# Optimization experiments

Hardware: AMD Instinct MI355X
Metric: run time of the kernel (lower is better)

## Reference

```python
import jax, jax.numpy as jnp
import numpy as np

DIM = 128
HEADS = 4
HD = DIM // HEADS  # 32
WS = 8             # search window (ws x ws candidates)
K = 16             # top-k neighbors kept
SCALE = HD ** -0.5


def _sepconv(x, w_dw, w_pw, b):
    # depthwise 3x3 ('SAME', reflect-free) + pointwise 1x1 with bias (SepConv2d)
    C = x.shape[1]
    y = jax.lax.conv_general_dilated(x, w_dw, (1, 1), 'SAME',
                                     feature_group_count=C,
                                     dimension_numbers=('NCHW', 'OIHW', 'NCHW'))
    return jnp.einsum('bchw,oc->bohw', y, w_pw) + b[None, :, None, None]


def _refl(i, n):
    # dnls reflect_bounds: mirror indices back into [0, n-1]
    i = jnp.where(i < 0, -i, i)
    return jnp.where(i >= n, 2 * (n - 1) - i, i)


def _neighbor_idx(T, H, W, ws):
    # flat pixel index of the ws*ws spatial candidates per query (wt=0: same frame)
    off = jnp.arange(ws) - ws // 2
    ni = _refl(jnp.arange(H)[:, None] + off[None, :], H)  # [H,ws]
    nj = _refl(jnp.arange(W)[:, None] + off[None, :], W)  # [W,ws]
    pix = ni[:, None, :, None] * W + nj[None, :, None, :]  # [H,W,ws,ws]
    idx = jnp.arange(T)[:, None, None, None, None] * (H * W) + pix[None]
    return idx.reshape(T * H * W, ws * ws).astype(jnp.int32)  # [Q,L]


def reference(vid, wq_dw, wq_pw, bq, wk_dw, wk_pw, bk, wv_dw, wv_pw, bv, proj_w, proj_b):
    B, T, C, H, W = vid.shape
    Q = T * H * W
    x = vid.reshape(B * T, C, H, W)
    # qkv conv projection; q pre-scaled as in get_qkv
    q = _sepconv(x, wq_dw, wq_pw, bq) * SCALE
    k = _sepconv(x, wk_dw, wk_pw, bk)
    v = _sepconv(x, wv_dw, wv_pw, bv)

    def heads(z):  # [B*T,C,H,W] -> [B,heads,Q,hd]
        return z.reshape(B, T, HEADS, HD, H, W).transpose(0, 2, 1, 4, 5, 3).reshape(B, HEADS, Q, HD)

    qh, kh, vh = heads(q), heads(k), heads(v)
    idx = _neighbor_idx(T, H, W, WS)            # [Q,L]
    kg = jnp.take(kh, idx, axis=2)              # [B,h,Q,L,hd] irregular gather
    dists = jnp.einsum('bhqd,bhqld->bhql', qh, kg)
    vals, args = jax.lax.top_k(dists, K)        # k-NN by prod distance
    attn = jax.nn.softmax(vals, axis=-1)        # run_softmax over k
    sel = jnp.take_along_axis(jnp.broadcast_to(idx[None, None], (B, HEADS) + idx.shape), args, axis=-1)
    vsel = jnp.take_along_axis(vh, sel.reshape(B, HEADS, Q * K)[..., None], axis=2).reshape(B, HEADS, Q, K, HD)
    out = jnp.einsum('bhqk,bhqkd->bhqd', attn, vsel)   # wpsum (ps=pt=1)
    out = out.transpose(0, 2, 1, 3).reshape(B, Q, C)   # merge heads: (h c)
    y = out @ proj_w.T + proj_b                        # nn.Linear proj
    # fold: ps=1, stride0=1 -> zvid==1, pure reshape back to video
    return y.reshape(B, T, H, W, C).transpose(0, 1, 4, 2, 3)


def setup_inputs() -> dict:
    key = jax.random.key(0)
    ks = jax.random.split(key, 12)
    s = 0.02
    return {
        'vid': jax.random.normal(ks[0], (1, 2, DIM, 96, 96), jnp.float32),
        'wq_dw': jax.random.normal(ks[1], (DIM, 1, 3, 3), jnp.float32) * s,
        'wq_pw': jax.random.normal(ks[2], (DIM, DIM), jnp.float32) * s,
        'bq': jax.random.normal(ks[3], (DIM,), jnp.float32) * s,
        'wk_dw': jax.random.normal(ks[4], (DIM, 1, 3, 3), jnp.float32) * s,
        'wk_pw': jax.random.normal(ks[5], (DIM, DIM), jnp.float32) * s,
        'bk': jax.random.normal(ks[6], (DIM,), jnp.float32) * s,
        'wv_dw': jax.random.normal(ks[7], (DIM, 1, 3, 3), jnp.float32) * s,
        'wv_pw': jax.random.normal(ks[8], (DIM, DIM), jnp.float32) * s,
        'bv': jax.random.normal(ks[9], (DIM,), jnp.float32) * s,
        'proj_w': jax.random.normal(ks[10], (DIM, DIM), jnp.float32) * s,
        'proj_b': jax.random.normal(ks[11], (DIM,), jnp.float32) * s,
    }
```

## Files before the change

### kernel.cpp

```cpp
#include <hip/hip_runtime.h>
#include <math.h>

#define TT 2
#define CH 128
#define HH 96
#define WW 96
#define HWS 9216
#define QTOT 18432
#define QC (QTOT*CH)
#define HD 32
#define KTOP 16
#define SCALE 0.17677669529663687f

#define SEG 16
#define PR 8
#define PC 23
#define PSTRIDE 36

typedef __attribute__((ext_vector_type(8))) short short8;
typedef __attribute__((ext_vector_type(4))) float floatx4;

__device__ __forceinline__ unsigned short f2bf(float f) {
    union { float f; unsigned u; } x; x.f = f;
    unsigned r = x.u + 0x7fffu + ((x.u >> 16) & 1u);
    return (unsigned short)(r >> 16);
}
__device__ __forceinline__ float bf2f(unsigned short h) {
    return __uint_as_float(((unsigned)h) << 16);
}

__device__ __forceinline__ int refl(int x, int n) {
    x = x < 0 ? -x : x;
    return x >= n ? 2 * (n - 1) - x : x;
}

__global__ __launch_bounds__(256) void dwcvt_kernel(
    const float* __restrict__ x,
    const float* __restrict__ wq, const float* __restrict__ wk, const float* __restrict__ wv,
    unsigned short* __restrict__ qk_hi,
    unsigned short* __restrict__ qk_lo,
    unsigned short* __restrict__ v_bf)
{
    int t = threadIdx.x;
    int pl = t & 63;
    int cg = __builtin_amdgcn_readfirstlane(t >> 6);
    int p  = blockIdx.x * 64 + pl;
    int c0 = blockIdx.y * 32 + cg * 8;
    int hw = p % HWS;
    int tt = p / HWS;
    int i = hw / WW, j = hw % WW;

    unsigned qh[4], ql[4], kh[4], kl[4], vh4[4];
#pragma unroll
    for (int ic = 0; ic < 8; ic += 2) {
        float sv[3][2];
#pragma unroll
        for (int u = 0; u < 2; u++) {
            int c = c0 + ic + u;
            const float* xp = x + (size_t)(tt * CH + c) * HWS;
            float w0[9], w1[9], w2[9];
#pragma unroll
            for (int r = 0; r < 9; r++) {
                w0[r] = wq[c * 9 + r]; w1[r] = wk[c * 9 + r]; w2[r] = wv[c * 9 + r];
            }
            float s0 = 0.f, s1 = 0.f, s2 = 0.f;
#pragma unroll
            for (int r = 0; r < 3; r++) {
                int ii = i + r - 1;
                if (ii < 0 || ii >= HH) continue;
#pragma unroll
                for (int ss = 0; ss < 3; ss++) {
                    int jj = j + ss - 1;
                    if (jj < 0 || jj >= WW) continue;
                    float xv = xp[ii * WW + jj];
                    s0 += xv * w0[r * 3 + ss];
                    s1 += xv * w1[r * 3 + ss];
                    s2 += xv * w2[r * 3 + ss];
                }
            }
            sv[0][u] = s0; sv[1][u] = s1; sv[2][u] = s2;
        }
        int w = ic >> 1;
        unsigned short h0 = f2bf(sv[0][0]), h1 = f2bf(sv[0][1]);
        qh[w] = h0 | ((unsigned)h1 << 16);
        ql[w] = f2bf(sv[0][0] - bf2f(h0)) | ((unsigned)f2bf(sv[0][1] - bf2f(h1)) << 16);
        h0 = f2bf(sv[1][0]); h1 = f2bf(sv[1][1]);
        kh[w] = h0 | ((unsigned)h1 << 16);
        kl[w] = f2bf(sv[1][0] - bf2f(h0)) | ((unsigned)f2bf(sv[1][1] - bf2f(h1)) << 16);
        vh4[w] = f2bf(sv[2][0]) | ((unsigned)f2bf(sv[2][1]) << 16);
    }
    size_t off = (size_t)p * CH + c0;
    uint4 pk;
    pk.x = qh[0]; pk.y = qh[1]; pk.z = qh[2]; pk.w = qh[3];
    *(uint4*)(qk_hi + off) = pk;
    pk.x = ql[0]; pk.y = ql[1]; pk.z = ql[2]; pk.w = ql[3];
    *(uint4*)(qk_lo + off) = pk;
    pk.x = kh[0]; pk.y = kh[1]; pk.z = kh[2]; pk.w = kh[3];
    *(uint4*)(qk_hi + (size_t)QC + off) = pk;
    pk.x = kl[0]; pk.y = kl[1]; pk.z = kl[2]; pk.w = kl[3];
    *(uint4*)(qk_lo + (size_t)QC + off) = pk;
    pk.x = vh4[0]; pk.y = vh4[1]; pk.z = vh4[2]; pk.w = vh4[3];
    *(uint4*)(v_bf + off) = pk;
}

__global__ __launch_bounds__(256) void qkv_mfma(
    const unsigned short* __restrict__ Ahi,
    const unsigned short* __restrict__ Alo,
    const unsigned short* __restrict__ Avb,
    const float* __restrict__ wq_pw, const float* __restrict__ wk_pw,
    const float* __restrict__ wv_pw,
    const float* __restrict__ bq, const float* __restrict__ bk, const float* __restrict__ bv,
    float* __restrict__ qkf,
    unsigned short* __restrict__ vh)
{
    __shared__ unsigned short WhS[128 * 136];
    __shared__ unsigned short WlS[128 * 136];
    int sel = blockIdx.y;
    int t = threadIdx.x;
    int wv = t >> 6, lane = t & 63;
    int m = lane & 15, quad = lane >> 4;
    int p0 = blockIdx.x * 64;
    int o0 = wv * 32;

    if (sel == 2) {
#pragma unroll
        for (int r = 0; r < 16; r++) {
            int lin = r * 256 + t;
            int o = lin >> 5, cq = lin & 31;
            float4 w4 = *(const float4*)(wv_pw + o * CH + cq * 4);
            uint2 pk;
            pk.x = f2bf(w4.x) | ((unsigned)f2bf(w4.y) << 16);
            pk.y = f2bf(w4.z) | ((unsigned)f2bf(w4.w) << 16);
            *(uint2*)(&WhS[o * 136 + cq * 4]) = pk;
        }
        __syncthreads();
        float bb[2];
#pragma unroll
        for (int ot = 0; ot < 2; ot++) bb[ot] = bv[o0 + ot * 16 + m];
        floatx4 acc[4][2];
#pragma unroll
        for (int i = 0; i < 4; i++)
#pragma unroll
            for (int j = 0; j < 2; j++) acc[i][j] = (floatx4){0.f, 0.f, 0.f, 0.f};
#pragma unroll
        for (int kc = 0; kc < 4; kc++) {
            short8 a[4], b[2];
#pragma unroll
            for (int pt = 0; pt < 4; pt++)
                a[pt] = *(const short8*)(Avb + (size_t)(p0 + pt * 16 + m) * CH + kc * 32 + quad * 8);
#pragma unroll
            for (int ot = 0; ot < 2; ot++)
                b[ot] = *(const short8*)(&WhS[(o0 + ot * 16 + m) * 136 + kc * 32 + quad * 8]);
#pragma unroll
            for (int pt = 0; pt < 4; pt++)
#pragma unroll
                for (int ot = 0; ot < 2; ot++)
                    acc[pt][ot] = __builtin_amdgcn_mfma_f32_16x16x32_bf16(a[pt], b[ot], acc[pt][ot], 0, 0, 0);
        }
        unsigned short* vhh = vh + (size_t)wv * QTOT * 32;
#pragma unroll
        for (int pt = 0; pt < 4; pt++)
#pragma unroll
            for (int ot = 0; ot < 2; ot++)
#pragma unroll
                for (int reg = 0; reg < 4; reg++) {
                    int p = p0 + pt * 16 + quad * 4 + reg;
                    vhh[(size_t)p * 32 + ot * 16 + m] = f2bf(acc[pt][ot][reg] + bb[ot]);
                }
        return;
    }

    const float* W = sel ? wk_pw : wq_pw;
    const float* bias = sel ? bk : bq;
    float scale = sel ? 1.f : SCALE;
    const unsigned short* ah = Ahi + (size_t)sel * QC;
    const unsigned short* al = Alo + (size_t)sel * QC;
    float* O = qkf + (size_t)sel * QC;

#pragma unroll
    for (int r = 0; r < 16; r++) {
        int lin = r * 256 + t;
        int o = lin >> 5, cq = lin & 31;
        float4 w4 = *(const float4*)(W + o * CH + cq * 4);
        unsigned short hx = f2bf(w4.x), hy = f2bf(w4.y), hz = f2bf(w4.z), hw = f2bf(w4.w);
        unsigned short lx = f2bf(w4.x - bf2f(hx)), ly = f2bf(w4.y - bf2f(hy));
        unsigned short lz = f2bf(w4.z - bf2f(hz)), lw = f2bf(w4.w - bf2f(hw));
        uint2 pk;
        pk.x = hx | ((unsigned)hy << 16); pk.y = hz | ((unsigned)hw << 16);
        *(uint2*)(&WhS[o * 136 + cq * 4]) = pk;
        pk.x = lx | ((unsigned)ly << 16); pk.y = lz | ((unsigned)lw << 16);
        *(uint2*)(&WlS[o * 136 + cq * 4]) = pk;
    }
    __syncthreads();
    float bb[2];
#pragma unroll
    for (int ot = 0; ot < 2; ot++) bb[ot] = bias[o0 + ot * 16 + m];
    floatx4 acc[4][2];
#pragma unroll
    for (int i = 0; i < 4; i++)
#pragma unroll
        for (int j = 0; j < 2; j++) acc[i][j] = (floatx4){0.f, 0.f, 0.f, 0.f};
#pragma unroll
    for (int kc = 0; kc < 4; kc++) {
        short8 avh[4], avl[4], bh[2], bl[2];
#pragma unroll
        for (int pt = 0; pt < 4; pt++) {
            size_t base = (size_t)(p0 + pt * 16 + m) * CH + kc * 32 + quad * 8;
            avh[pt] = *(const short8*)(ah + base);
            avl[pt] = *(const short8*)(al + base);
        }
#pragma unroll
        for (int ot = 0; ot < 2; ot++) {
            int lidx = (o0 + ot * 16 + m) * 136 + kc * 32 + quad * 8;
            bh[ot] = *(const short8*)(&WhS[lidx]);
            bl[ot] = *(const short8*)(&WlS[lidx]);
        }
#pragma unroll
        for (int pt = 0; pt < 4; pt++)
#pragma unroll
            for (int ot = 0; ot < 2; ot++) {
                acc[pt][ot] = __builtin_amdgcn_mfma_f32_16x16x32_bf16(avh[pt], bh[ot], acc[pt][ot], 0, 0, 0);
                acc[pt][ot] = __builtin_amdgcn_mfma_f32_16x16x32_bf16(avh[pt], bl[ot], acc[pt][ot], 0, 0, 0);
                acc[pt][ot] = __builtin_amdgcn_mfma_f32_16x16x32_bf16(avl[pt], bh[ot], acc[pt][ot], 0, 0, 0);
            }
    }
#pragma unroll
    for (int pt = 0; pt < 4; pt++)
#pragma unroll
        for (int ot = 0; ot < 2; ot++)
#pragma unroll
            for (int reg = 0; reg < 4; reg++) {
                int p = p0 + pt * 16 + quad * 4 + reg;
                O[(size_t)p * CH + o0 + ot * 16 + m] = (acc[pt][ot][reg] + bb[ot]) * scale;
            }
}

__global__ __launch_bounds__(256) void attn_kernel(
    const float* __restrict__ q,
    const float* __restrict__ k,
    const unsigned short* __restrict__ vh,
    unsigned short* __restrict__ att)
{
    __shared__ float kp[PR * PC * PSTRIDE];
    int h = blockIdx.y;
    int n = blockIdx.x;
    int seg = (n & 7) * 144 + (n >> 3);
    int qj0 = (seg % (WW / SEG)) * SEG;
    int qi = (seg / (WW / SEG)) % HH;
    int tt = seg / ((WW / SEG) * HH);
    int t = threadIdx.x;

#pragma unroll
    for (int r = 0; r < 6; r++) {
        int f = r * 256 + t;
        if (f < PR * PC * 8) {
            int pix = f >> 3, d4 = f & 7;
            int ci = pix / PC, cj = pix - ci * PC;
            int gi = refl(qi + ci - 4, HH);
            int gj = refl(qj0 + cj - 4, WW);
            int gp = tt * HWS + gi * WW + gj;
            *(float4*)(&kp[pix * PSTRIDE + d4 * 4]) =
                *(const float4*)(k + (size_t)gp * CH + h * HD + d4 * 4);
        }
    }
    __syncthreads();

    int wv = t >> 6, lane = t & 63;
    int ci = lane >> 3, cjo = lane & 7;
    int di = ci - 4, dj = cjo - 4;
    int rowoff = tt * HWS + refl(qi + di, HH) * WW;
    const int d = lane & (HD - 1);
    const unsigned long long below = (1ull << lane) - 1ull;
    const unsigned short* vhh = vh + (size_t)h * QTOT * 32;

    for (int ql = wv * 4; ql < wv * 4 + 4; ql++) {
        int qj = qj0 + ql;
        int p = tt * HWS + qi * WW + qj;
        const float* qp = q + (size_t)p * CH + h * HD;
        const float* kr = &kp[(ci * PC + ql + cjo) * PSTRIDE];
        float dist = 0.f;
#pragma unroll
        for (int dd = 0; dd < 8; dd++) {
            float4 qv = *(const float4*)(qp + dd * 4);
            float4 kv = *(const float4*)(kr + dd * 4);
            dist += qv.x * kv.x + qv.y * kv.y + qv.z * kv.z + qv.w * kv.w;
        }
        int cpix = rowoff + refl(qj + dj, WW);

        unsigned u = __float_as_uint(dist);
        unsigned key = (u & 0x80000000u) ? ~u : (u | 0x80000000u);

        unsigned prefix = 0u;
        int need = KTOP;
#pragma unroll
        for (int bit = 31; bit >= 0; --bit) {
            unsigned hi = (prefix >> bit) | 1u;
            unsigned long long b = __ballot((key >> bit) == hi);
            int cnt = __popcll(b);
            bool take = cnt >= need;
            prefix = take ? (prefix | (1u << bit)) : prefix;
            need = take ? need : need - cnt;
        }
        bool isEq = (key == prefix);
        unsigned long long eqm = __ballot(isEq);
        int rk = __popcll(eqm & below);
        bool selb = (key > prefix) || (isEq && rk < need);
        unsigned long long selm = __ballot(selb);

        float e = selb ? __expf(dist) : 0.f;

        float acc = 0.f, denom = 0.f;
        unsigned long long m0 = selm;
#pragma unroll
        for (int r = 0; r < KTOP; r++) {
            int s0 = __builtin_ctzll(m0); m0 &= m0 - 1ull;
            float a0 = __uint_as_float((unsigned)__builtin_amdgcn_readlane((int)__float_as_uint(e), s0));
            int pr = __builtin_amdgcn_readlane(cpix, s0);
            denom += a0;
            acc += a0 * bf2f(vhh[(size_t)pr * 32 + d]);
        }
        if (lane < HD)
            att[(size_t)p * CH + h * HD + lane] = f2bf(acc / denom);
    }
}

__global__ __launch_bounds__(256) void proj_mfma(
    const unsigned short* __restrict__ A,
    const float* __restrict__ W,
    const float* __restrict__ bias,
    float* __restrict__ out)
{
    __shared__ unsigned short Ws[128 * 136];
    int t = threadIdx.x;
#pragma unroll
    for (int r = 0; r < 16; r++) {
        int lin = r * 256 + t;
        int o = lin >> 5, cq = lin & 31;
        float4 w4 = *(const float4*)(W + o * CH + cq * 4);
        uint2 pk;
        pk.x = f2bf(w4.x) | ((unsigned)f2bf(w4.y) << 16);
        pk.y = f2bf(w4.z) | ((unsigned)f2bf(w4.w) << 16);
        *(uint2*)(&Ws[o * 136 + cq * 4]) = pk;
    }
    __syncthreads();
    int wv = t >> 6, lane = t & 63;
    int m = lane & 15, quad = lane >> 4;
    int p0 = blockIdx.x * 64;
    int o0 = wv * 32;
    float bb[2][4];
#pragma unroll
    for (int ot = 0; ot < 2; ot++)
#pragma unroll
        for (int reg = 0; reg < 4; reg++) bb[ot][reg] = bias[o0 + ot * 16 + quad * 4 + reg];
    floatx4 acc[2][4];
#pragma unroll
    for (int i = 0; i < 2; i++)
#pragma unroll
        for (int j = 0; j < 4; j++) acc[i][j] = (floatx4){0.f, 0.f, 0.f, 0.f};
#pragma unroll
    for (int kc = 0; kc < 4; kc++) {
        short8 a[2], b[4];
#pragma unroll
        for (int ot = 0; ot < 2; ot++)
            a[ot] = *(const short8*)(&Ws[(o0 + ot * 16 + m) * 136 + kc * 32 + quad * 8]);
#pragma unroll
        for (int pt = 0; pt < 4; pt++)
            b[pt] = *(const short8*)(A + (size_t)(p0 + pt * 16 + m) * CH + kc * 32 + quad * 8);
#pragma unroll
        for (int ot = 0; ot < 2; ot++)
#pragma unroll
            for (int pt = 0; pt < 4; pt++)
                acc[ot][pt] = __builtin_amdgcn_mfma_f32_16x16x32_bf16(a[ot], b[pt], acc[ot][pt], 0, 0, 0);
    }
    int tt = p0 / HWS;
    int hwb = p0 - tt * HWS;
#pragma unroll
    for (int ot = 0; ot < 2; ot++)
#pragma unroll
        for (int pt = 0; pt < 4; pt++)
#pragma unroll
            for (int reg = 0; reg < 4; reg++) {
                int o = o0 + ot * 16 + quad * 4 + reg;
                int hw = hwb + pt * 16 + m;
                out[((size_t)(tt * CH + o)) * HWS + hw] = acc[ot][pt][reg] + bb[ot][reg];
            }
}

extern "C" void kernel_launch(void* const* d_in, const int* in_sizes, int n_in,
                              void* d_out, int out_size, void* d_ws, size_t ws_size,
                              hipStream_t stream) {
    const float* vid    = (const float*)d_in[0];
    const float* wq_dw  = (const float*)d_in[1];
    const float* wq_pw  = (const float*)d_in[2];
    const float* bq     = (const float*)d_in[3];
    const float* wk_dw  = (const float*)d_in[4];
    const float* wk_pw  = (const float*)d_in[5];
    const float* bk     = (const float*)d_in[6];
    const float* wv_dw  = (const float*)d_in[7];
    const float* wv_pw  = (const float*)d_in[8];
    const float* bv     = (const float*)d_in[9];
    const float* proj_w = (const float*)d_in[10];
    const float* proj_b = (const float*)d_in[11];
    float* out = (float*)d_out;

    float* qkf = (float*)d_ws;
    unsigned short* vh = (unsigned short*)(qkf + (size_t)2 * QC);
    unsigned short* qk_hi = vh + (size_t)QC;
    unsigned short* qk_lo = qk_hi + (size_t)2 * QC;
    unsigned short* v_bf = qk_lo + (size_t)2 * QC;
    unsigned short* att_bf = v_bf;

    dwcvt_kernel<<<dim3(QTOT / 64, 4), 256, 0, stream>>>(
        vid, wq_dw, wk_dw, wv_dw, qk_hi, qk_lo, v_bf);
    qkv_mfma<<<dim3(QTOT / 64, 3), 256, 0, stream>>>(
        qk_hi, qk_lo, v_bf, wq_pw, wk_pw, wv_pw, bq, bk, bv, qkf, vh);
    attn_kernel<<<dim3(TT * HH * (WW / SEG), 4), 256, 0, stream>>>(
        qkf, qkf + (size_t)QC, vh, att_bf);
    proj_mfma<<<QTOT / 64, 256, 0, stream>>>(att_bf, proj_w, proj_b, out);
}
```

Baseline: 203.6 us.

## Precompute bf16 weight splits once and compact top-k selection via LDS slots

Adds an extra block column to the depthwise kernel that converts all pointwise and projection weights to bf16 hi/lo once into a workspace buffer. The GEMM kernels then copy ready-made bf16 weights into LDS instead of each block redoing the float-to-bf16 split. In the attention kernel, selected top-k entries are written to a per-wave LDS slot array using mbcnt ranks, replacing the serial ctz/readlane loop. The risk is that the extra LDS traffic and the dependency on the new workspace region may offset the savings.

```diff
diff --git a/kernel.cpp b/kernel.cpp
--- a/kernel.cpp
+++ b/kernel.cpp
@@ -17,6 +17,8 @@
 #define PC 23
 #define PSTRIDE 36
 
+#define WB_TOT 98304
+
 typedef __attribute__((ext_vector_type(8))) short short8;
 typedef __attribute__((ext_vector_type(4))) float floatx4;
 
@@ -37,11 +39,36 @@
 __global__ __launch_bounds__(256) void dwcvt_kernel(
     const float* __restrict__ x,
     const float* __restrict__ wq, const float* __restrict__ wk, const float* __restrict__ wv,
+    const float* __restrict__ wq_pw, const float* __restrict__ wk_pw,
+    const float* __restrict__ wv_pw, const float* __restrict__ proj_w,
     unsigned short* __restrict__ qk_hi,
     unsigned short* __restrict__ qk_lo,
-    unsigned short* __restrict__ v_bf)
+    unsigned short* __restrict__ v_bf,
+    unsigned short* __restrict__ wbuf)
 {
     int t = threadIdx.x;
+    if (blockIdx.x == 288) {
+        int y = blockIdx.y;
+        const float* src = y == 0 ? wq_pw : (y == 1 ? wk_pw : (y == 2 ? wv_pw : proj_w));
+        unsigned short* hi = wbuf + (y == 0 ? 0 : (y == 1 ? 32768 : (y == 2 ? 65536 : 81920)));
+#pragma unroll
+        for (int r = 0; r < 16; r++) {
+            int idx = r * 256 + t;
+            float4 w4 = *(const float4*)(src + idx * 4);
+            unsigned short hx = f2bf(w4.x), hy = f2bf(w4.y), hz = f2bf(w4.z), hw = f2bf(w4.w);
+            uint2 pk;
+            pk.x = hx | ((unsigned)hy << 16); pk.y = hz | ((unsigned)hw << 16);
+            *(uint2*)(hi + idx * 4) = pk;
+            if (y < 2) {
+                unsigned short lx = f2bf(w4.x - bf2f(hx)), ly = f2bf(w4.y - bf2f(hy));
+                unsigned short lz = f2bf(w4.z - bf2f(hz)), lw = f2bf(w4.w - bf2f(hw));
+                pk.x = lx | ((unsigned)ly << 16); pk.y = lz | ((unsigned)lw << 16);
+                *(uint2*)(hi + 16384 + idx * 4) = pk;
+            }
+        }
+        return;
+    }
+
     int pl = t & 63;
     int cg = __builtin_amdgcn_readfirstlane(t >> 6);
     int p  = blockIdx.x * 64 + pl;
@@ -107,8 +134,7 @@
     const unsigned short* __restrict__ Ahi,
     const unsigned short* __restrict__ Alo,
     const unsigned short* __restrict__ Avb,
-    const float* __restrict__ wq_pw, const float* __restrict__ wk_pw,
-    const float* __restrict__ wv_pw,
+    const unsigned short* __restrict__ wbuf,
     const float* __restrict__ bq, const float* __restrict__ bk, const float* __restrict__ bv,
     float* __restrict__ qkf,
     unsigned short* __restrict__ vh)
@@ -123,15 +149,12 @@
     int o0 = wv * 32;
 
     if (sel == 2) {
+        const unsigned short* Wg = wbuf + 65536;
 #pragma unroll
         for (int r = 0; r < 16; r++) {
             int lin = r * 256 + t;
             int o = lin >> 5, cq = lin & 31;
-            float4 w4 = *(const float4*)(wv_pw + o * CH + cq * 4);
-            uint2 pk;
-            pk.x = f2bf(w4.x) | ((unsigned)f2bf(w4.y) << 16);
-            pk.y = f2bf(w4.z) | ((unsigned)f2bf(w4.w) << 16);
-            *(uint2*)(&WhS[o * 136 + cq * 4]) = pk;
+            *(uint2*)(&WhS[o * 136 + cq * 4]) = *(const uint2*)(Wg + o * CH + cq * 4);
         }
         __syncthreads();
         float bb[2];
@@ -170,7 +193,8 @@
         return;
     }
 
-    const float* W = sel ? wk_pw : wq_pw;
+    const unsigned short* Wh_g = wbuf + sel * 32768;
+    const unsigned short* Wl_g = Wh_g + 16384;
     const float* bias = sel ? bk : bq;
     float scale = sel ? 1.f : SCALE;
     const unsigned short* ah = Ahi + (size_t)sel * QC;
@@ -181,15 +205,8 @@
     for (int r = 0; r < 16; r++) {
         int lin = r * 256 + t;
         int o = lin >> 5, cq = lin & 31;
-        float4 w4 = *(const float4*)(W + o * CH + cq * 4);
-        unsigned short hx = f2bf(w4.x), hy = f2bf(w4.y), hz = f2bf(w4.z), hw = f2bf(w4.w);
-        unsigned short lx = f2bf(w4.x - bf2f(hx)), ly = f2bf(w4.y - bf2f(hy));
-        unsigned short lz = f2bf(w4.z - bf2f(hz)), lw = f2bf(w4.w - bf2f(hw));
-        uint2 pk;
-        pk.x = hx | ((unsigned)hy << 16); pk.y = hz | ((unsigned)hw << 16);
-        *(uint2*)(&WhS[o * 136 + cq * 4]) = pk;
-        pk.x = lx | ((unsigned)ly << 16); pk.y = lz | ((unsigned)lw << 16);
-        *(uint2*)(&WlS[o * 136 + cq * 4]) = pk;
+        *(uint2*)(&WhS[o * 136 + cq * 4]) = *(const uint2*)(Wh_g + o * CH + cq * 4);
+        *(uint2*)(&WlS[o * 136 + cq * 4]) = *(const uint2*)(Wl_g + o * CH + cq * 4);
     }
     __syncthreads();
     float bb[2];
@@ -242,6 +259,7 @@
     unsigned short* __restrict__ att)
 {
     __shared__ float kp[PR * PC * PSTRIDE];
+    __shared__ uint2 slot[4][16];
     int h = blockIdx.y;
     int n = blockIdx.x;
     int seg = (n & 7) * 144 + (n >> 3);
@@ -263,9 +281,11 @@
                 *(const float4*)(k + (size_t)gp * CH + h * HD + d4 * 4);
         }
     }
+
+    int wv = t >> 6, lane = t & 63;
+    if (lane < KTOP) slot[wv][lane] = make_uint2(0u, 0u);
     __syncthreads();
 
-    int wv = t >> 6, lane = t & 63;
     int ci = lane >> 3, cjo = lane & 7;
     int di = ci - 4, dj = cjo - 4;
     int rowoff = tt * HWS + refl(qi + di, HH) * WW;
@@ -309,15 +329,17 @@
 
         float e = selb ? __expf(dist) : 0.f;
 
+        int rksel = __builtin_amdgcn_mbcnt_hi(
+            (unsigned)(selm >> 32), __builtin_amdgcn_mbcnt_lo((unsigned)selm, 0));
+        if (selb && rksel < KTOP) slot[wv][rksel] = make_uint2(__float_as_uint(e), (unsigned)cpix);
+
         float acc = 0.f, denom = 0.f;
-        unsigned long long m0 = selm;
 #pragma unroll
         for (int r = 0; r < KTOP; r++) {
-            int s0 = __builtin_ctzll(m0); m0 &= m0 - 1ull;
-            float a0 = __uint_as_float((unsigned)__builtin_amdgcn_readlane((int)__float_as_uint(e), s0));
-            int pr = __builtin_amdgcn_readlane(cpix, s0);
+            uint2 sp = slot[wv][r];
+            float a0 = __uint_as_float(sp.x);
             denom += a0;
-            acc += a0 * bf2f(vhh[(size_t)pr * 32 + d]);
+            acc += a0 * bf2f(vhh[(size_t)sp.y * 32 + d]);
         }
         if (lane < HD)
             att[(size_t)p * CH + h * HD + lane] = f2bf(acc / denom);
@@ -326,21 +348,18 @@
 
 __global__ __launch_bounds__(256) void proj_mfma(
     const unsigned short* __restrict__ A,
-    const float* __restrict__ W,
+    const unsigned short* __restrict__ wbuf,
     const float* __restrict__ bias,
     float* __restrict__ out)
 {
     __shared__ unsigned short Ws[128 * 136];
+    const unsigned short* Wg = wbuf + 81920;
     int t = threadIdx.x;
 #pragma unroll
     for (int r = 0; r < 16; r++) {
         int lin = r * 256 + t;
         int o = lin >> 5, cq = lin & 31;
-        float4 w4 = *(const float4*)(W + o * CH + cq * 4);
-        uint2 pk;
-        pk.x = f2bf(w4.x) | ((unsigned)f2bf(w4.y) << 16);
-        pk.y = f2bf(w4.z) | ((unsigned)f2bf(w4.w) << 16);
-        *(uint2*)(&Ws[o * 136 + cq * 4]) = pk;
+        *(uint2*)(&Ws[o * 136 + cq * 4]) = *(const uint2*)(Wg + o * CH + cq * 4);
     }
     __syncthreads();
     int wv = t >> 6, lane = t & 63;
@@ -408,13 +427,15 @@
     unsigned short* qk_hi = vh + (size_t)QC;
     unsigned short* qk_lo = qk_hi + (size_t)2 * QC;
     unsigned short* v_bf = qk_lo + (size_t)2 * QC;
+    unsigned short* wbuf = v_bf + (size_t)QC;
     unsigned short* att_bf = v_bf;
 
-    dwcvt_kernel<<<dim3(QTOT / 64, 4), 256, 0, stream>>>(
-        vid, wq_dw, wk_dw, wv_dw, qk_hi, qk_lo, v_bf);
+    dwcvt_kernel<<<dim3(289, 4), 256, 0, stream>>>(
+        vid, wq_dw, wk_dw, wv_dw, wq_pw, wk_pw, wv_pw, proj_w,
+        qk_hi, qk_lo, v_bf, wbuf);
     qkv_mfma<<<dim3(QTOT / 64, 3), 256, 0, stream>>>(
-        qk_hi, qk_lo, v_bf, wq_pw, wk_pw, wv_pw, bq, bk, bv, qkf, vh);
+        qk_hi, qk_lo, v_bf, wbuf, bq, bk, bv, qkf, vh);
     attn_kernel<<<dim3(TT * HH * (WW / SEG), 4), 256, 0, stream>>>(
         qkf, qkf + (size_t)QC, vh, att_bf);
-    proj_mfma<<<QTOT / 64, 256, 0, stream>>>(att_bf, proj_w, proj_b, out);
-}
+    proj_mfma<<<QTOT / 64, 256, 0, stream>>>(att_bf, wbuf, proj_b, out);
+}
```

New measurement: 192.9 us (median of 2 runs). 5.3% less time.
